# Kernel optimization log

Measured on AMD Instinct MI355X. Metric: run time of the kernel, lower is better.

## Reference

```python
import jax, jax.numpy as jnp
import numpy as np

EPS = 1e-9
NUM_GATES = 64
SECOND_THRESHOLD = 0.2  # eval threshold (module defaults train==eval)
CAPACITY_FACTOR = 1.25
MIN_EXPERT_CAPACITY = 4


def setup_inputs() -> dict:
    key = jax.random.key(0)
    k1, k2, k3 = jax.random.split(key, 3)
    b, n, d = 8, 2048, 1024
    x = jax.random.normal(k1, (b, n, d), dtype=jnp.float32)
    w_gating = jax.random.normal(k2, (d, NUM_GATES), dtype=jnp.float32)
    uniform_noise = jax.random.uniform(k3, (b, n), dtype=jnp.float32)
    return {"x": x, "w_gating": w_gating, "uniform_noise": uniform_noise}


def reference(x, w_gating, uniform_noise):
    b, n, d = x.shape
    e = NUM_GATES
    dt = x.dtype

    # raw gates: small matmul + softmax over experts
    raw_gates = jax.nn.softmax(jnp.einsum('bnd,de->bne', x, w_gating), axis=-1)

    # top-1 expert
    gate_1 = jnp.max(raw_gates, axis=-1)            # [b, n]
    index_1 = jnp.argmax(raw_gates, axis=-1)        # [b, n]
    mask_1 = jax.nn.one_hot(index_1, e, dtype=dt)   # [b, n, e]
    density_1_proxy = raw_gates

    # top-2 expert (top-1 of gates with top-1 removed)
    gates_wo1 = raw_gates * (1.0 - mask_1)
    gate_2 = jnp.max(gates_wo1, axis=-1)
    index_2 = jnp.argmax(gates_wo1, axis=-1)
    mask_2 = jax.nn.one_hot(index_2, e, dtype=dt)

    # renormalize top-2 gate values
    denom = gate_1 + gate_2 + EPS
    gate_1 = gate_1 / denom
    gate_2 = gate_2 / denom

    # load-balancing loss
    density_1 = jnp.mean(mask_1, axis=-2)                 # [b, e]
    loss = jnp.mean(jnp.mean(density_1_proxy, axis=-2) * density_1) * float(e * e)

    # second policy == 'random': route to 2nd expert with prob ~ gate_2 / threshold
    keep2 = (uniform_noise < (gate_2 / max(SECOND_THRESHOLD, EPS))).astype(dt)
    mask_2 = mask_2 * keep2[..., None]

    # static expert capacity
    cap = max(min(n, int((n * 2) / e * CAPACITY_FACTOR)), MIN_EXPERT_CAPACITY)
    capf = float(cap)

    # exclusive cumsum over tokens -> position of each token within its expert
    pos1 = (jnp.cumsum(mask_1, axis=-2) - mask_1) * mask_1        # [b, n, e]
    mask_1 = mask_1 * (pos1 < capf).astype(dt)
    mask_1_count = jnp.sum(mask_1, axis=-2, keepdims=True)        # [b, 1, e]
    mask_1_flat = jnp.sum(mask_1, axis=-1)                        # [b, n]
    pos1 = jnpp_sum = jnp.sum(pos1, axis=-1)                      # [b, n]
    gate_1 = gate_1 * mask_1_flat

    pos2 = (jnp.cumsum(mask_2, axis=-2) - mask_2) + mask_1_count
    pos2 = pos2 * mask_2
    mask_2 = mask_2 * (pos2 < capf).astype(dt)
    mask_2_flat = jnp.sum(mask_2, axis=-1)
    pos2 = jnp.sum(pos2, axis=-1)
    gate_2 = gate_2 * mask_2_flat

    # combine tensor [b, n, e, cap]; out-of-range positions one-hot to zero
    oh_e1 = jax.nn.one_hot(index_1, e, dtype=dt)
    oh_e2 = jax.nn.one_hot(index_2, e, dtype=dt)
    oh_c1 = jax.nn.one_hot(pos1.astype(jnp.int32), cap, dtype=dt)
    oh_c2 = jax.nn.one_hot(pos2.astype(jnp.int32), cap, dtype=dt)
    combine = (gate_1[..., None, None] * oh_e1[..., :, None] * oh_c1[..., None, :]
               + gate_2[..., None, None] * oh_e2[..., :, None] * oh_c2[..., None, :])
    dispatch = (combine > 0).astype(dt)
    return dispatch, combine, loss
```

## Files before the change

kernel.cpp:

```cpp
#include <hip/hip_runtime.h>
#include <math.h>

#define NTOK 16384
#define NPB  2048
#define DDIM 1024
#define NEXP 64
#define CAP  80
#define ROWF 5120
#define SOUT 83886080LL

typedef float vf4 __attribute__((ext_vector_type(4)));

#define OFF_ROUTE  0
#define OFF_POS1   (OFF_ROUTE + NTOK*4)
#define OFF_POS2   (OFF_POS1  + NTOK*4)
#define OFF_CNT1   (OFF_POS2  + NTOK*4)
#define OFF_PART   (OFF_CNT1  + 2048)
#define OFF_G12    (OFF_PART  + 65536)

__global__ __launch_bounds__(256) void k_gate(
    const float* __restrict__ x, const float* __restrict__ w,
    const float* __restrict__ noise,
    int* __restrict__ route, float2* __restrict__ g12,
    float* __restrict__ part)
{
    __shared__ float xs[32][68];
    __shared__ float wl[32][64];
    __shared__ float lg[64][68];
    __shared__ float sG[4][64];

    const int tid  = threadIdx.x;
    const int tok0 = blockIdx.x * 64;
    const int tx = tid & 15, ty = tid >> 4;
    float acc[4][4] = {{0.f}};

    const float* xb = x + (size_t)tok0 * DDIM;
    const int t0 = tid >> 3, c0 = (tid & 7) * 4;

    float4 px0 = *(const float4*)(xb + (size_t)t0 * DDIM + c0);
    float4 px1 = *(const float4*)(xb + (size_t)(t0 + 32) * DDIM + c0);
    float4 pw0 = ((const float4*)w)[tid];
    float4 pw1 = ((const float4*)w)[tid + 256];

    for (int k0 = 0; k0 < DDIM; k0 += 32) {
        xs[c0+0][t0] = px0.x; xs[c0+1][t0] = px0.y;
        xs[c0+2][t0] = px0.z; xs[c0+3][t0] = px0.w;
        xs[c0+0][t0+32] = px1.x; xs[c0+1][t0+32] = px1.y;
        xs[c0+2][t0+32] = px1.z; xs[c0+3][t0+32] = px1.w;
        ((float4*)wl)[tid]       = pw0;
        ((float4*)wl)[tid + 256] = pw1;
        __syncthreads();

        if (k0 + 32 < DDIM) {
            px0 = *(const float4*)(xb + (size_t)t0 * DDIM + k0 + 32 + c0);
            px1 = *(const float4*)(xb + (size_t)(t0 + 32) * DDIM + k0 + 32 + c0);
            const float4* wp = (const float4*)(w + (size_t)(k0 + 32) * NEXP);
            pw0 = wp[tid];
            pw1 = wp[tid + 256];
        }

        #pragma unroll
        for (int k = 0; k < 32; ++k) {
            float4 a  = *(const float4*)&xs[k][ty * 4];
            float4 bb = *(const float4*)&wl[k][tx * 4];
            float av[4] = {a.x, a.y, a.z, a.w};
            float bv[4] = {bb.x, bb.y, bb.z, bb.w};
            #pragma unroll
            for (int i = 0; i < 4; ++i)
                #pragma unroll
                for (int j = 0; j < 4; ++j)
                    acc[i][j] = fmaf(av[i], bv[j], acc[i][j]);
        }
        __syncthreads();
    }

    #pragma unroll
    for (int i = 0; i < 4; ++i)
        *(float4*)&lg[ty * 4 + i][tx * 4] =
            make_float4(acc[i][0], acc[i][1], acc[i][2], acc[i][3]);
    __syncthreads();

    const int lane = tid & 63;
    const int wv   = tid >> 6;
    float gsum_acc = 0.f;

    for (int it = 0; it < 16; ++it) {
        int t = wv * 16 + it;
        float v = lg[t][lane];

        float m = v; int mi = lane;
        #pragma unroll
        for (int off = 32; off; off >>= 1) {
            float ov = __shfl_xor(m, off, 64);
            int   oi = __shfl_xor(mi, off, 64);
            if (ov > m || (ov == m && oi < mi)) { m = ov; mi = oi; }
        }
        float v2 = (lane == mi) ? -INFINITY : v;
        float m2 = v2; int mi2 = lane;
        #pragma unroll
        for (int off = 32; off; off >>= 1) {
            float ov = __shfl_xor(m2, off, 64);
            int   oi = __shfl_xor(mi2, off, 64);
            if (ov > m2 || (ov == m2 && oi < mi2)) { m2 = ov; mi2 = oi; }
        }
        float ex = expf(v - m);
        float s = ex;
        #pragma unroll
        for (int off = 32; off; off >>= 1) s += __shfl_xor(s, off, 64);

        float inv   = 1.0f / s;
        float gate1 = inv;
        float gate2 = expf(m2 - m) * inv;
        gsum_acc += ex * inv;

        float denom = gate1 + gate2 + 1e-9f;
        float g1n = gate1 / denom;
        float g2n = gate2 / denom;

        int gt = tok0 + t;
        if (lane == 0) {
            float u = noise[gt];
            int k2 = (u < (g2n / 0.2f)) ? 1 : 0;
            route[gt] = mi | (mi2 << 8) | (k2 << 16);
            g12[gt] = make_float2(g1n, g2n);
        }
    }

    sG[wv][lane] = gsum_acc;
    __syncthreads();
    if (tid < 64)
        part[blockIdx.x * 64 + tid] =
            sG[0][tid] + sG[1][tid] + sG[2][tid] + sG[3][tid];
}

__global__ __launch_bounds__(256) void k_pos(
    const int* __restrict__ route,
    int* __restrict__ pos1, int* __restrict__ pos2raw,
    int* __restrict__ cnt1tot)
{
    const int b    = blockIdx.x;
    const int tid  = threadIdx.x;
    const int lane = tid & 63, wv = tid >> 6;
    __shared__ int sr[NPB];
    __shared__ int h1[32][64], h2[32][64];

    for (int i = tid; i < NPB; i += 256) sr[i] = route[b * NPB + i];
    __syncthreads();

    for (int tau = wv; tau < 32; tau += 4) {
        int c1 = 0, c2 = 0;
        const int* p = &sr[tau * 64];
        #pragma unroll 8
        for (int j = 0; j < 64; ++j) {
            int r = p[j];
            c1 += ((r & 255) == lane);
            c2 += ((r >> 16) && (((r >> 8) & 255) == lane));
        }
        h1[tau][lane] = c1; h2[tau][lane] = c2;
    }
    __syncthreads();

    if (tid < 64) {
        int run = 0;
        #pragma unroll 8
        for (int tau = 0; tau < 32; ++tau) {
            int t = h1[tau][tid]; h1[tau][tid] = run; run += t;
        }
        cnt1tot[b * NEXP + tid] = run;
    } else if (tid < 128) {
        int e = tid - 64, run = 0;
        #pragma unroll 8
        for (int tau = 0; tau < 32; ++tau) {
            int t = h2[tau][e]; h2[tau][e] = run; run += t;
        }
    }
    __syncthreads();

    for (int tau = wv; tau < 32; tau += 4) {
        int c1 = h1[tau][lane], c2 = h2[tau][lane];
        const int* p = &sr[tau * 64];
        const int gbase = b * NPB + tau * 64;
        #pragma unroll 4
        for (int j = 0; j < 64; ++j) {
            int r = p[j];
            if ((r & 255) == lane) pos1[gbase + j] = c1++;
            if ((r >> 16) && (((r >> 8) & 255) == lane)) pos2raw[gbase + j] = c2++;
        }
    }
}

__global__ __launch_bounds__(256) void k_out(
    const int* __restrict__ route,
    const int* __restrict__ pos1, const int* __restrict__ pos2raw,
    const int* __restrict__ cnt1tot,
    const float2* __restrict__ g12, const float* __restrict__ part,
    float* __restrict__ out)
{
    const int tid = threadIdx.x;
    const int bid = blockIdx.x;

    if (bid == 4096) {
        __shared__ float red[4];
        float v = 0.f;
        for (int p = tid; p < 512; p += 256) {
            int b = p >> 6, e = p & 63;
            float s = 0.f;
            #pragma unroll 8
            for (int c = 0; c < 32; ++c) s += part[((b << 5) + c) * 64 + e];
            v += s * (float)cnt1tot[p];
        }
        #pragma unroll
        for (int off = 32; off; off >>= 1) v += __shfl_xor(v, off, 64);
        if ((tid & 63) == 0) red[tid >> 6] = v;
        __syncthreads();
        if (tid == 0)
            out[2 * SOUT] = (red[0] + red[1] + red[2] + red[3]) * (1.0f / 524288.0f);
        return;
    }

    const int tg = bid * 4;

    __shared__ int   se[4][2];
    __shared__ float sv[4][2];

    if (tid < 4) {
        int t = tg + tid;
        int b = t >> 11;
        int r  = route[t];
        int i1 = r & 255, i2 = (r >> 8) & 255, k2 = (r >> 16);
        float2 g = g12[t];

        int p1 = pos1[t];
        se[tid][0] = (p1 < CAP) ? (i1 * CAP + p1) : -1;
        sv[tid][0] = g.x;

        int e2 = -1;
        if (k2) {
            int m1c = min(cnt1tot[(b << 6) + i2], CAP);
            int p2  = pos2raw[t] + m1c;
            if (p2 < CAP) e2 = i2 * CAP + p2;
        }
        se[tid][1] = e2;
        sv[tid][1] = g.y;
    }
    __syncthreads();

    vf4* dbase = (vf4*)(out + (size_t)tg * ROWF);
    vf4* cbase = (vf4*)(out + (size_t)SOUT + (size_t)tg * ROWF);
    #pragma unroll
    for (int t = 0; t < 4; ++t) {
        const int   e1 = se[t][0], e2 = se[t][1];
        const float v1 = sv[t][0], v2 = sv[t][1];
        const int   q1 = e1 >> 2, q2 = e2 >> 2;
        vf4* pd = dbase + (size_t)t * (ROWF / 4);
        vf4* pc = cbase + (size_t)t * (ROWF / 4);
        for (int s = tid; s < ROWF / 4; s += 256) {
            vf4 d = {0.f, 0.f, 0.f, 0.f};
            vf4 c = {0.f, 0.f, 0.f, 0.f};
            if (s == q1) { d[e1 & 3] = 1.f; c[e1 & 3] = v1; }
            if (s == q2) { d[e2 & 3] = 1.f; c[e2 & 3] = v2; }
            __builtin_nontemporal_store(d, pd + s);
            __builtin_nontemporal_store(c, pc + s);
        }
    }
}

extern "C" void kernel_launch(void* const* d_in, const int* in_sizes, int n_in,
                              void* d_out, int out_size, void* d_ws, size_t ws_size,
                              hipStream_t stream) {
    (void)in_sizes; (void)n_in; (void)ws_size; (void)out_size;
    const float* x     = (const float*)d_in[0];
    const float* w     = (const float*)d_in[1];
    const float* noise = (const float*)d_in[2];
    float* out = (float*)d_out;
    char*  ws  = (char*)d_ws;

    int*    route   = (int*)   (ws + OFF_ROUTE);
    int*    pos1    = (int*)   (ws + OFF_POS1);
    int*    pos2raw = (int*)   (ws + OFF_POS2);
    int*    cnt1tot = (int*)   (ws + OFF_CNT1);
    float*  part    = (float*) (ws + OFF_PART);
    float2* g12     = (float2*)(ws + OFF_G12);

    k_gate<<<dim3(NTOK / 64), dim3(256), 0, stream>>>(
        x, w, noise, route, g12, part);
    k_pos<<<dim3(8), dim3(256), 0, stream>>>(
        route, pos1, pos2raw, cnt1tot);
    k_out<<<dim3(4097), dim3(256), 0, stream>>>(
        route, pos1, pos2raw, cnt1tot, g12, part, out);
}
```

Baseline: 800.4 us.

## Restructure gating GEMM into single-wave 32-token blocks with packed FMA

```diff
diff --git a/kernel.cpp b/kernel.cpp
--- a/kernel.cpp
+++ b/kernel.cpp
@@ -10,82 +10,84 @@
 #define SOUT 83886080LL
 
 typedef float vf4 __attribute__((ext_vector_type(4)));
+typedef float vf2 __attribute__((ext_vector_type(2)));
 
 #define OFF_ROUTE  0
 #define OFF_POS1   (OFF_ROUTE + NTOK*4)
 #define OFF_POS2   (OFF_POS1  + NTOK*4)
 #define OFF_CNT1   (OFF_POS2  + NTOK*4)
 #define OFF_PART   (OFF_CNT1  + 2048)
-#define OFF_G12    (OFF_PART  + 65536)
-
-__global__ __launch_bounds__(256) void k_gate(
+#define OFF_G12    (OFF_PART  + 131072)
+
+__global__ __launch_bounds__(64) void k_gate(
     const float* __restrict__ x, const float* __restrict__ w,
     const float* __restrict__ noise,
     int* __restrict__ route, float2* __restrict__ g12,
     float* __restrict__ part)
 {
-    __shared__ float xs[32][68];
-    __shared__ float wl[32][64];
-    __shared__ float lg[64][68];
-    __shared__ float sG[4][64];
-
-    const int tid  = threadIdx.x;
-    const int tok0 = blockIdx.x * 64;
-    const int tx = tid & 15, ty = tid >> 4;
-    float acc[4][4] = {{0.f}};
+    __shared__ float xs[64][36];
+    __shared__ float lg[32][65];
+
+    const int lane = threadIdx.x;
+    const int tok0 = blockIdx.x * 32;
+    const int tt = lane >> 4;
+    const int tx = lane & 15;
+    const int st = lane >> 1, sh = lane & 1;
+
+    vf2 acc[4][4] = {};
 
     const float* xb = x + (size_t)tok0 * DDIM;
-    const int t0 = tid >> 3, c0 = (tid & 7) * 4;
-
-    float4 px0 = *(const float4*)(xb + (size_t)t0 * DDIM + c0);
-    float4 px1 = *(const float4*)(xb + (size_t)(t0 + 32) * DDIM + c0);
-    float4 pw0 = ((const float4*)w)[tid];
-    float4 pw1 = ((const float4*)w)[tid + 256];
-
-    for (int k0 = 0; k0 < DDIM; k0 += 32) {
-        xs[c0+0][t0] = px0.x; xs[c0+1][t0] = px0.y;
-        xs[c0+2][t0] = px0.z; xs[c0+3][t0] = px0.w;
-        xs[c0+0][t0+32] = px1.x; xs[c0+1][t0+32] = px1.y;
-        xs[c0+2][t0+32] = px1.z; xs[c0+3][t0+32] = px1.w;
-        ((float4*)wl)[tid]       = pw0;
-        ((float4*)wl)[tid + 256] = pw1;
+
+    float4 px[8];
+    #pragma unroll
+    for (int r = 0; r < 8; ++r)
+        px[r] = *(const float4*)(xb + (size_t)st * DDIM + (sh * 8 + r) * 4);
+
+    for (int k0 = 0; k0 < DDIM; k0 += 64) {
+        #pragma unroll
+        for (int r = 0; r < 8; ++r) {
+            int kk = (sh * 8 + r) * 4;
+            xs[kk+0][st] = px[r].x; xs[kk+1][st] = px[r].y;
+            xs[kk+2][st] = px[r].z; xs[kk+3][st] = px[r].w;
+        }
         __syncthreads();
 
-        if (k0 + 32 < DDIM) {
-            px0 = *(const float4*)(xb + (size_t)t0 * DDIM + k0 + 32 + c0);
-            px1 = *(const float4*)(xb + (size_t)(t0 + 32) * DDIM + k0 + 32 + c0);
-            const float4* wp = (const float4*)(w + (size_t)(k0 + 32) * NEXP);
-            pw0 = wp[tid];
-            pw1 = wp[tid + 256];
-        }
-
-        #pragma unroll
-        for (int k = 0; k < 32; ++k) {
-            float4 a  = *(const float4*)&xs[k][ty * 4];
-            float4 bb = *(const float4*)&wl[k][tx * 4];
-            float av[4] = {a.x, a.y, a.z, a.w};
+        if (k0 + 64 < DDIM) {
+            #pragma unroll
+            for (int r = 0; r < 8; ++r)
+                px[r] = *(const float4*)(xb + (size_t)st * DDIM + k0 + 64 + (sh * 8 + r) * 4);
+        }
+
+        const float* wk = w + (size_t)k0 * NEXP + tx * 4;
+        #pragma unroll 8
+        for (int k = 0; k < 64; ++k) {
+            vf4 aA = *(const vf4*)&xs[k][tt * 8];
+            vf4 aB = *(const vf4*)&xs[k][tt * 8 + 4];
+            float4 bb = *(const float4*)(wk + (size_t)k * NEXP);
+            vf2 a2[4] = {{aA.x, aA.y}, {aA.z, aA.w}, {aB.x, aB.y}, {aB.z, aB.w}};
             float bv[4] = {bb.x, bb.y, bb.z, bb.w};
             #pragma unroll
-            for (int i = 0; i < 4; ++i)
+            for (int p = 0; p < 4; ++p)
                 #pragma unroll
-                for (int j = 0; j < 4; ++j)
-                    acc[i][j] = fmaf(av[i], bv[j], acc[i][j]);
+                for (int j = 0; j < 4; ++j) {
+                    vf2 b2 = {bv[j], bv[j]};
+                    acc[p][j] += a2[p] * b2;
+                }
         }
         __syncthreads();
     }
 
     #pragma unroll
-    for (int i = 0; i < 4; ++i)
-        *(float4*)&lg[ty * 4 + i][tx * 4] =
-            make_float4(acc[i][0], acc[i][1], acc[i][2], acc[i][3]);
-    __syncthreads();
-
-    const int lane = tid & 63;
-    const int wv   = tid >> 6;
+    for (int p = 0; p < 4; ++p)
+        #pragma unroll
+        for (int j = 0; j < 4; ++j) {
+            lg[tt * 8 + p * 2 + 0][tx * 4 + j] = acc[p][j].x;
+            lg[tt * 8 + p * 2 + 1][tx * 4 + j] = acc[p][j].y;
+        }
+    __syncthreads();
+
     float gsum_acc = 0.f;
-
-    for (int it = 0; it < 16; ++it) {
-        int t = wv * 16 + it;
+    for (int t = 0; t < 32; ++t) {
         float v = lg[t][lane];
 
         float m = v; int mi = lane;
@@ -126,11 +128,7 @@
         }
     }
 
-    sG[wv][lane] = gsum_acc;
-    __syncthreads();
-    if (tid < 64)
-        part[blockIdx.x * 64 + tid] =
-            sG[0][tid] + sG[1][tid] + sG[2][tid] + sG[3][tid];
+    part[blockIdx.x * 64 + lane] = gsum_acc;
 }
 
 __global__ __launch_bounds__(256) void k_pos(
@@ -206,7 +204,7 @@
             int b = p >> 6, e = p & 63;
             float s = 0.f;
             #pragma unroll 8
-            for (int c = 0; c < 32; ++c) s += part[((b << 5) + c) * 64 + e];
+            for (int c = 0; c < 64; ++c) s += part[((b << 6) + c) * 64 + e];
             v += s * (float)cnt1tot[p];
         }
         #pragma unroll
@@ -282,7 +280,7 @@
     float*  part    = (float*) (ws + OFF_PART);
     float2* g12     = (float2*)(ws + OFF_G12);
 
-    k_gate<<<dim3(NTOK / 64), dim3(256), 0, stream>>>(
+    k_gate<<<dim3(NTOK / 32), dim3(64), 0, stream>>>(
         x, w, noise, route, g12, part);
     k_pos<<<dim3(8), dim3(256), 0, stream>>>(
         route, pos1, pos2raw, cnt1tot);
```

After: 1.184 ms. 47.9% more time.

## Replace LDS-tiled gating GEMM with per-wave register GEMM over 8 tokens

Applied to the files above, without the earlier changes.

```diff
diff --git a/kernel.cpp b/kernel.cpp
--- a/kernel.cpp
+++ b/kernel.cpp
@@ -16,7 +16,7 @@
 #define OFF_POS2   (OFF_POS1  + NTOK*4)
 #define OFF_CNT1   (OFF_POS2  + NTOK*4)
 #define OFF_PART   (OFF_CNT1  + 2048)
-#define OFF_G12    (OFF_PART  + 65536)
+#define OFF_G12    (OFF_PART  + 131072)
 
 __global__ __launch_bounds__(256) void k_gate(
     const float* __restrict__ x, const float* __restrict__ w,
@@ -24,69 +24,32 @@
     int* __restrict__ route, float2* __restrict__ g12,
     float* __restrict__ part)
 {
-    __shared__ float xs[32][68];
-    __shared__ float wl[32][64];
-    __shared__ float lg[64][68];
     __shared__ float sG[4][64];
-
     const int tid  = threadIdx.x;
-    const int tok0 = blockIdx.x * 64;
-    const int tx = tid & 15, ty = tid >> 4;
-    float acc[4][4] = {{0.f}};
-
+    const int lane = tid & 63;
+    const int wv   = __builtin_amdgcn_readfirstlane(tid >> 6);
+    const int tok0 = blockIdx.x * 32 + wv * 8;
     const float* xb = x + (size_t)tok0 * DDIM;
-    const int t0 = tid >> 3, c0 = (tid & 7) * 4;
-
-    float4 px0 = *(const float4*)(xb + (size_t)t0 * DDIM + c0);
-    float4 px1 = *(const float4*)(xb + (size_t)(t0 + 32) * DDIM + c0);
-    float4 pw0 = ((const float4*)w)[tid];
-    float4 pw1 = ((const float4*)w)[tid + 256];
-
-    for (int k0 = 0; k0 < DDIM; k0 += 32) {
-        xs[c0+0][t0] = px0.x; xs[c0+1][t0] = px0.y;
-        xs[c0+2][t0] = px0.z; xs[c0+3][t0] = px0.w;
-        xs[c0+0][t0+32] = px1.x; xs[c0+1][t0+32] = px1.y;
-        xs[c0+2][t0+32] = px1.z; xs[c0+3][t0+32] = px1.w;
-        ((float4*)wl)[tid]       = pw0;
-        ((float4*)wl)[tid + 256] = pw1;
-        __syncthreads();
-
-        if (k0 + 32 < DDIM) {
-            px0 = *(const float4*)(xb + (size_t)t0 * DDIM + k0 + 32 + c0);
-            px1 = *(const float4*)(xb + (size_t)(t0 + 32) * DDIM + k0 + 32 + c0);
-            const float4* wp = (const float4*)(w + (size_t)(k0 + 32) * NEXP);
-            pw0 = wp[tid];
-            pw1 = wp[tid + 256];
-        }
-
-        #pragma unroll
-        for (int k = 0; k < 32; ++k) {
-            float4 a  = *(const float4*)&xs[k][ty * 4];
-            float4 bb = *(const float4*)&wl[k][tx * 4];
-            float av[4] = {a.x, a.y, a.z, a.w};
-            float bv[4] = {bb.x, bb.y, bb.z, bb.w};
+
+    float acc[8] = {0.f, 0.f, 0.f, 0.f, 0.f, 0.f, 0.f, 0.f};
+
+    for (int k0 = 0; k0 < DDIM; k0 += 8) {
+        float wr[8];
+        #pragma unroll
+        for (int j = 0; j < 8; ++j)
+            wr[j] = w[(size_t)(k0 + j) * NEXP + lane];
+        #pragma unroll
+        for (int t = 0; t < 8; ++t) {
             #pragma unroll
-            for (int i = 0; i < 4; ++i)
-                #pragma unroll
-                for (int j = 0; j < 4; ++j)
-                    acc[i][j] = fmaf(av[i], bv[j], acc[i][j]);
-        }
-        __syncthreads();
-    }
-
+            for (int j = 0; j < 8; ++j)
+                acc[t] = fmaf(xb[(size_t)t * DDIM + k0 + j], wr[j], acc[t]);
+        }
+    }
+
+    float gsum_acc = 0.f;
     #pragma unroll
-    for (int i = 0; i < 4; ++i)
-        *(float4*)&lg[ty * 4 + i][tx * 4] =
-            make_float4(acc[i][0], acc[i][1], acc[i][2], acc[i][3]);
-    __syncthreads();
-
-    const int lane = tid & 63;
-    const int wv   = tid >> 6;
-    float gsum_acc = 0.f;
-
-    for (int it = 0; it < 16; ++it) {
-        int t = wv * 16 + it;
-        float v = lg[t][lane];
+    for (int t = 0; t < 8; ++t) {
+        float v = acc[t];
 
         float m = v; int mi = lane;
         #pragma unroll
@@ -206,7 +169,7 @@
             int b = p >> 6, e = p & 63;
             float s = 0.f;
             #pragma unroll 8
-            for (int c = 0; c < 32; ++c) s += part[((b << 5) + c) * 64 + e];
+            for (int c = 0; c < 64; ++c) s += part[((b << 6) + c) * 64 + e];
             v += s * (float)cnt1tot[p];
         }
         #pragma unroll
@@ -282,7 +245,7 @@
     float*  part    = (float*) (ws + OFF_PART);
     float2* g12     = (float2*)(ws + OFF_G12);
 
-    k_gate<<<dim3(NTOK / 64), dim3(256), 0, stream>>>(
+    k_gate<<<dim3(NTOK / 32), dim3(256), 0, stream>>>(
         x, w, noise, route, g12, part);
     k_pos<<<dim3(8), dim3(256), 0, stream>>>(
         route, pos1, pos2raw, cnt1tot);
```

Result: slower. 866.3 us (+8.2%).
